# Kernel optimization log

Hardware: AMD Instinct MI355X
Metric: run time of the kernel (lower is better)

## Reference

```python
import jax, jax.numpy as jnp
import numpy as np

N_NODES = 100000
N_EDGES = 1200000
NUM_GRAPHS = 128
IN_DIM = 5
HIDDEN = 64


def setup_inputs() -> dict:
    key = jax.random.key(0)
    ks = jax.random.split(key, 12)
    x = jax.random.normal(ks[0], (N_NODES, IN_DIM), dtype=jnp.float32)
    edge_index = jax.random.randint(ks[1], (2, N_EDGES), 0, N_NODES, dtype=jnp.int64 if jax.config.read('jax_enable_x64') else jnp.int32)
    batch = jnp.sort(jax.random.randint(ks[2], (N_NODES,), 0, NUM_GRAPHS, dtype=jnp.int32))
    s = lambda fan_in: 1.0 / np.sqrt(fan_in)
    return {
        'x': x,
        'edge_index': edge_index,
        'batch': batch,
        'w_rel1': jax.random.normal(ks[3], (IN_DIM, HIDDEN), dtype=jnp.float32) * s(IN_DIM),
        'b_rel1': jnp.zeros((HIDDEN,), dtype=jnp.float32),
        'w_root1': jax.random.normal(ks[4], (IN_DIM, HIDDEN), dtype=jnp.float32) * s(IN_DIM),
        'w_rel2': jax.random.normal(ks[5], (HIDDEN, HIDDEN), dtype=jnp.float32) * s(HIDDEN),
        'b_rel2': jnp.zeros((HIDDEN,), dtype=jnp.float32),
        'w_root2': jax.random.normal(ks[6], (HIDDEN, HIDDEN), dtype=jnp.float32) * s(HIDDEN),
        'w_h1': jax.random.normal(ks[7], (2 * HIDDEN, HIDDEN), dtype=jnp.float32) * s(2 * HIDDEN),
        'b_h1': jnp.zeros((HIDDEN,), dtype=jnp.float32),
        'w_h2': jax.random.normal(ks[8], (HIDDEN, 1), dtype=jnp.float32) * s(HIDDEN),
        'b_h2': jnp.zeros((1,), dtype=jnp.float32),
    }


def _graph_conv(x, src, dst, w_rel, b_rel, w_root):
    # PyG GraphConv (aggr='add'): out = aggr(x_src -> dst) @ W_rel + b_rel + x @ W_root
    agg = jax.ops.segment_sum(x[src], dst, num_segments=N_NODES)
    return agg @ w_rel + b_rel + x @ w_root


def reference(x, edge_index, batch,
              w_rel1, b_rel1, w_root1,
              w_rel2, b_rel2, w_root2,
              w_h1, b_h1, w_h2, b_h2):
    src, dst = edge_index[0], edge_index[1]
    h = jax.nn.relu(_graph_conv(x, src, dst, w_rel1, b_rel1, w_root1))
    h = jax.nn.relu(_graph_conv(h, src, dst, w_rel2, b_rel2, w_root2))
    # global add + mean pooling over graphs
    add_pool = jax.ops.segment_sum(h, batch, num_segments=NUM_GRAPHS)
    counts = jax.ops.segment_sum(jnp.ones((N_NODES,), h.dtype), batch, num_segments=NUM_GRAPHS)
    mean_pool = add_pool / jnp.maximum(counts, 1.0)[:, None]
    g = jnp.concatenate([mean_pool, add_pool], axis=1)  # [G, 2*HIDDEN]
    out = jax.nn.relu(g @ w_h1 + b_h1) @ w_h2 + b_h2
    return out.squeeze(-1)
```

## Files before the change

### kernel.cpp

```cpp
#include <hip/hip_runtime.h>
#include <hip/hip_bf16.h>

#define N_NODES    100000
#define N_EDGES    1200000
#define NUM_GRAPHS 128
#define IN_DIM     5
#define HIDDEN     64
#define M_TILES    (N_NODES / 16)
#define NI4        (N_EDGES / 4)

#define CB    782
#define CBLK  256
#define EPB   ((NI4 + CBLK - 1) / CBLK)

typedef __attribute__((ext_vector_type(8))) short short8;
typedef __attribute__((ext_vector_type(4))) float f32x4;

__device__ __forceinline__ int rfl(int v) { return __builtin_amdgcn_readfirstlane(v); }

__device__ __forceinline__ unsigned short f2bs(float f) {
    union { float f; unsigned u; } v; v.f = f;
    return (unsigned short)((v.u + 0x7FFFu + ((v.u >> 16) & 1u)) >> 16);
}
__device__ __forceinline__ float bs2f(unsigned short s) {
    union { unsigned u; float f; } v; v.u = ((unsigned)s) << 16;
    return v.f;
}
__device__ __forceinline__ float blo(unsigned p) { return bs2f((unsigned short)(p & 0xffff)); }
__device__ __forceinline__ float bhi(unsigned p) { return bs2f((unsigned short)(p >> 16)); }
__device__ __forceinline__ unsigned pack2(float a, float b) {
    return ((unsigned)f2bs(b) << 16) | (unsigned)f2bs(a);
}

__device__ __forceinline__ unsigned char f2f8(float f) {
    union { float f; unsigned u; } v; v.f = f * 0x1p-120f;
    unsigned u = v.u + 0x7FFFFu + ((v.u >> 20) & 1u);
    return (unsigned char)(u >> 20);
}
__device__ __forceinline__ float f82f(unsigned b) {
    union { unsigned u; float f; } v; v.u = (b & 0x7Fu) << 20;
    return v.f * 0x1p120f;
}


__global__ void coarse_count(const int* __restrict__ dst, int* __restrict__ gcnt) {
    __shared__ int h[CB];
    int t = threadIdx.x, b = blockIdx.x;
    for (int i = t; i < CB; i += 256) h[i] = 0;
    __syncthreads();
    int i0 = b * EPB, i1 = min(i0 + EPB, NI4);
    for (int i = i0 + t; i < i1; i += 256) {
        int4 d = ((const int4*)dst)[i];
        atomicAdd(&h[d.x >> 7], 1);
        atomicAdd(&h[d.y >> 7], 1);
        atomicAdd(&h[d.z >> 7], 1);
        atomicAdd(&h[d.w >> 7], 1);
    }
    __syncthreads();
    for (int i = t; i < CB; i += 256) gcnt[b * CB + i] = h[i];
}

__global__ void block_scan(int* __restrict__ gcnt, int* __restrict__ btot) {
    __shared__ int s[CBLK];
    int k = blockIdx.x, t = threadIdx.x;
    int v = gcnt[t * CB + k];
    s[t] = v;
    __syncthreads();
    for (int off = 1; off < CBLK; off <<= 1) {
        int x = (t >= off) ? s[t - off] : 0;
        __syncthreads();
        s[t] += x;
        __syncthreads();
    }
    gcnt[t * CB + k] = s[t] - v;
    if (t == CBLK - 1) btot[k] = s[t];
}

__global__ void bucket_scan(const int* __restrict__ btot, int* __restrict__ bstart) {
    __shared__ int s[1024];
    int t = threadIdx.x;
    int v = (t < CB) ? btot[t] : 0;
    s[t] = v;
    __syncthreads();
    for (int off = 1; off < 1024; off <<= 1) {
        int x = (t >= off) ? s[t - off] : 0;
        __syncthreads();
        s[t] += x;
        __syncthreads();
    }
    if (t < CB) bstart[t] = s[t] - v;
    if (t == 0) bstart[CB] = N_EDGES;
}

__global__ void partition_k(const int* __restrict__ src, const int* __restrict__ dst,
                            const int* __restrict__ gcnt, const int* __restrict__ bstart,
                            int* __restrict__ part) {
    __shared__ int base[CB];
    __shared__ int h[CB];
    int t = threadIdx.x, b = blockIdx.x;
    for (int i = t; i < CB; i += 256) {
        base[i] = bstart[i] + gcnt[b * CB + i];
        h[i] = 0;
    }
    __syncthreads();
    int i0 = b * EPB, i1 = min(i0 + EPB, NI4);
    for (int i = i0 + t; i < i1; i += 256) {
        int4 s4 = ((const int4*)src)[i];
        int4 d4 = ((const int4*)dst)[i];
        int k, r;
        k = d4.x >> 7; r = atomicAdd(&h[k], 1); part[base[k] + r] = s4.x | ((d4.x & 127) << 17);
        k = d4.y >> 7; r = atomicAdd(&h[k], 1); part[base[k] + r] = s4.y | ((d4.y & 127) << 17);
        k = d4.z >> 7; r = atomicAdd(&h[k], 1); part[base[k] + r] = s4.z | ((d4.z & 127) << 17);
        k = d4.w >> 7; r = atomicAdd(&h[k], 1); part[base[k] + r] = s4.w | ((d4.w & 127) << 17);
    }
}

__global__ void fine_sort(const int* __restrict__ part, const int* __restrict__ bstart,
                          int* __restrict__ ptr, int* __restrict__ esrc) {
    __shared__ int fh[128];
    __shared__ int fr[128];
    int k = blockIdx.x, t = threadIdx.x;
    int e0 = bstart[k], e1 = bstart[k + 1];
    if (t < 128) { fh[t] = 0; fr[t] = 0; }
    __syncthreads();
    for (int e = e0 + t; e < e1; e += 256)
        atomicAdd(&fh[(part[e] >> 17) & 127], 1);
    __syncthreads();
    if (t == 0) {
        int run = 0;
        for (int i = 0; i < 128; ++i) { int c = fh[i]; fh[i] = run; run += c; }
    }
    __syncthreads();
    int n0 = k << 7;
    if (t < 128 && n0 + t < N_NODES) ptr[n0 + t] = e0 + fh[t];
    for (int e = e0 + t; e < e1; e += 256) {
        int p = part[e];
        int d = (p >> 17) & 127;
        int r = atomicAdd(&fr[d], 1);
        esrc[e0 + fh[d] + r] = p & 0x1FFFF;
    }
}


__global__ void packx_kernel(const float* __restrict__ x, uint4* __restrict__ xb) {
    int n = blockIdx.x * blockDim.x + threadIdx.x;
    if (n >= N_NODES) return;
    const float* xr = x + (size_t)n * IN_DIM;
    uint4 o;
    o.x = pack2(xr[0], xr[1]);
    o.y = pack2(xr[2], xr[3]);
    o.z = pack2(xr[4], 0.0f);
    o.w = 0u;
    xb[n] = o;
}

__global__ void gather_mlp1(const uint4* __restrict__ xb,
                            const float* __restrict__ x,
                            const int* __restrict__ ptr,
                            const int* __restrict__ esrc,
                            const float* __restrict__ w_rel1,
                            const float* __restrict__ b_rel1,
                            const float* __restrict__ w_root1,
                            unsigned short* __restrict__ h1,
                            unsigned char* __restrict__ h1f8) {
    int lane = threadIdx.x & 63;
    int w    = (blockIdx.x * blockDim.x + threadIdx.x) >> 6;
    int nw   = (gridDim.x * blockDim.x) >> 6;

    float wr[IN_DIM], wo[IN_DIM];
#pragma unroll
    for (int k = 0; k < IN_DIM; ++k) {
        wr[k] = w_rel1[k * HIDDEN + lane];
        wo[k] = w_root1[k * HIDDEN + lane];
    }
    float bias = b_rel1[lane];

    for (int n = w; n < N_NODES; n += nw) {
        int start = rfl(ptr[n]);
        int end   = rfl((n + 1 < N_NODES) ? ptr[n + 1] : N_EDGES);
        float a[IN_DIM] = {0.f, 0.f, 0.f, 0.f, 0.f};
        for (int e = start + lane; e < end; e += 64) {
            uint4 p = xb[esrc[e]];
            a[0] += blo(p.x); a[1] += bhi(p.x);
            a[2] += blo(p.y); a[3] += bhi(p.y);
            a[4] += blo(p.z);
        }
#pragma unroll
        for (int k = 0; k < IN_DIM; ++k)
#pragma unroll
            for (int off = 1; off < 64; off <<= 1)
                a[k] += __shfl_xor(a[k], off, 64);
        float acc = bias;
#pragma unroll
        for (int k = 0; k < IN_DIM; ++k)
            acc += a[k] * wr[k] + x[(size_t)n * IN_DIM + k] * wo[k];
        float hv = fmaxf(acc, 0.0f);
        h1[(size_t)n * HIDDEN + lane]   = f2bs(hv);
        h1f8[(size_t)n * HIDDEN + lane] = f2f8(hv);
    }
}

__global__ void gather2_fp8(const unsigned* __restrict__ h1f8,
                            const int* __restrict__ ptr,
                            const int* __restrict__ esrc,
                            uint2* __restrict__ agg2) {
    int lane = threadIdx.x & 63;
    int ql   = lane & 15;
    int q    = lane >> 4;
    int w    = (blockIdx.x * blockDim.x + threadIdx.x) >> 6;
    int nw   = (gridDim.x * blockDim.x) >> 6;

    for (int n = w; n < N_NODES; n += nw) {
        int start = rfl(ptr[n]);
        int end   = rfl((n + 1 < N_NODES) ? ptr[n + 1] : N_EDGES);
        float4 a0 = {0.f,0.f,0.f,0.f}, a1 = a0, a2 = a0, a3 = a0;
        int e = start + q;
        for (; e + 12 < end; e += 16) {
            int s0 = esrc[e], s1 = esrc[e + 4], s2 = esrc[e + 8], s3 = esrc[e + 12];
            unsigned p0 = h1f8[(size_t)s0 * 16 + ql];
            unsigned p1 = h1f8[(size_t)s1 * 16 + ql];
            unsigned p2 = h1f8[(size_t)s2 * 16 + ql];
            unsigned p3 = h1f8[(size_t)s3 * 16 + ql];
            a0.x += f82f(p0); a0.y += f82f(p0 >> 8); a0.z += f82f(p0 >> 16); a0.w += f82f(p0 >> 24);
            a1.x += f82f(p1); a1.y += f82f(p1 >> 8); a1.z += f82f(p1 >> 16); a1.w += f82f(p1 >> 24);
            a2.x += f82f(p2); a2.y += f82f(p2 >> 8); a2.z += f82f(p2 >> 16); a2.w += f82f(p2 >> 24);
            a3.x += f82f(p3); a3.y += f82f(p3 >> 8); a3.z += f82f(p3 >> 16); a3.w += f82f(p3 >> 24);
        }
        for (; e < end; e += 4) {
            unsigned p = h1f8[(size_t)esrc[e] * 16 + ql];
            a0.x += f82f(p); a0.y += f82f(p >> 8); a0.z += f82f(p >> 16); a0.w += f82f(p >> 24);
        }
        float4 a;
        a.x = (a0.x + a1.x) + (a2.x + a3.x);
        a.y = (a0.y + a1.y) + (a2.y + a3.y);
        a.z = (a0.z + a1.z) + (a2.z + a3.z);
        a.w = (a0.w + a1.w) + (a2.w + a3.w);
        a.x += __shfl_xor(a.x, 16, 64); a.x += __shfl_xor(a.x, 32, 64);
        a.y += __shfl_xor(a.y, 16, 64); a.y += __shfl_xor(a.y, 32, 64);
        a.z += __shfl_xor(a.z, 16, 64); a.z += __shfl_xor(a.z, 32, 64);
        a.w += __shfl_xor(a.w, 16, 64); a.w += __shfl_xor(a.w, 32, 64);
        if (q == 0) {
            uint2 o;
            o.x = pack2(a.x, a.y);
            o.y = pack2(a.z, a.w);
            agg2[(size_t)n * 16 + ql] = o;
        }
    }
}

__global__ void mlp2_pool(const unsigned short* __restrict__ agg2,
                          const unsigned short* __restrict__ h1,
                          const float* __restrict__ w_rel2,
                          const float* __restrict__ b_rel2,
                          const float* __restrict__ w_root2,
                          const int* __restrict__ batch,
                          float* __restrict__ add_pool) {
    int lane = threadIdx.x & 63;
    int wv   = threadIdx.x >> 6;
    int row  = lane & 15;
    int quad = lane >> 4;
    int n    = wv * 16 + row;

    short8 bwr[2], bwo[2];
#pragma unroll
    for (int s = 0; s < 2; ++s)
#pragma unroll
        for (int j = 0; j < 8; ++j) {
            int k = 32 * s + quad * 8 + j;
            bwr[s][j] = (short)f2bs(w_rel2[k * HIDDEN + n]);
            bwo[s][j] = (short)f2bs(w_root2[k * HIDDEN + n]);
        }
    float bias = b_rel2[n];

    for (int t = blockIdx.x; t < M_TILES; t += gridDim.x) {
        int m0 = t * 16;
        size_t rbase = (size_t)(m0 + row) * HIDDEN;
        short8 aa0 = *(const short8*)(agg2 + rbase + quad * 8);
        short8 aa1 = *(const short8*)(agg2 + rbase + 32 + quad * 8);
        short8 ah0 = *(const short8*)(h1   + rbase + quad * 8);
        short8 ah1 = *(const short8*)(h1   + rbase + 32 + quad * 8);

        f32x4 acc = {bias, bias, bias, bias};
        acc = __builtin_amdgcn_mfma_f32_16x16x32_bf16(aa0, bwr[0], acc, 0, 0, 0);
        acc = __builtin_amdgcn_mfma_f32_16x16x32_bf16(aa1, bwr[1], acc, 0, 0, 0);
        acc = __builtin_amdgcn_mfma_f32_16x16x32_bf16(ah0, bwo[0], acc, 0, 0, 0);
        acc = __builtin_amdgcn_mfma_f32_16x16x32_bf16(ah1, bwo[1], acc, 0, 0, 0);

        float hv0 = fmaxf(acc[0], 0.0f), hv1 = fmaxf(acc[1], 0.0f);
        float hv2 = fmaxf(acc[2], 0.0f), hv3 = fmaxf(acc[3], 0.0f);

        int gLo = batch[m0], gHi = batch[m0 + 15];
        if (gLo == gHi) {
            float s = (hv0 + hv1) + (hv2 + hv3);
            s += __shfl_xor(s, 16, 64);
            s += __shfl_xor(s, 32, 64);
            if (quad == 0)
                atomicAdd(&add_pool[gLo * HIDDEN + n], s);
        } else {
            int m = m0 + quad * 4;
            atomicAdd(&add_pool[batch[m]     * HIDDEN + n], hv0);
            atomicAdd(&add_pool[batch[m + 1] * HIDDEN + n], hv1);
            atomicAdd(&add_pool[batch[m + 2] * HIDDEN + n], hv2);
            atomicAdd(&add_pool[batch[m + 3] * HIDDEN + n], hv3);
        }
    }
}

__device__ __forceinline__ int lower_bound_i(const int* a, int n, int v) {
    int lo = 0, hi = n;
    while (lo < hi) { int mid = (lo + hi) >> 1; if (a[mid] < v) lo = mid + 1; else hi = mid; }
    return lo;
}

__global__ void head_mlp(const float* __restrict__ add_pool,
                         const int* __restrict__ batch,
                         const float* __restrict__ w_h1,
                         const float* __restrict__ b_h1,
                         const float* __restrict__ w_h2,
                         const float* __restrict__ b_h2,
                         float* __restrict__ out) {
    int g = blockIdx.x, t = threadIdx.x;

    __shared__ int s_cnt;
    if (t == 0) {
        int start = lower_bound_i(batch, N_NODES, g);
        int end   = lower_bound_i(batch, N_NODES, g + 1);
        s_cnt = end - start;
    }
    __syncthreads();
    float cnt = fmaxf((float)s_cnt, 1.0f);

    __shared__ float sg[2 * HIDDEN];
    float add = add_pool[(size_t)g * HIDDEN + t];
    sg[t]          = add / cnt;
    sg[HIDDEN + t] = add;
    __syncthreads();

    float hid = b_h1[t];
#pragma unroll 16
    for (int i = 0; i < 2 * HIDDEN; ++i)
        hid += sg[i] * w_h1[i * HIDDEN + t];
    hid = fmaxf(hid, 0.0f);

    float res = hid * w_h2[t];
    for (int off = 32; off > 0; off >>= 1)
        res += __shfl_down(res, off, 64);
    if (t == 0) out[g] = res + b_h2[0];
}

extern "C" void kernel_launch(void* const* d_in, const int* in_sizes, int n_in,
                              void* d_out, int out_size, void* d_ws, size_t ws_size,
                              hipStream_t stream) {
    const float* x       = (const float*)d_in[0];
    const int*   ei      = (const int*)d_in[1];
    const int*   src     = ei;
    const int*   dst     = ei + N_EDGES;
    const int*   batch   = (const int*)d_in[2];
    const float* w_rel1  = (const float*)d_in[3];
    const float* b_rel1  = (const float*)d_in[4];
    const float* w_root1 = (const float*)d_in[5];
    const float* w_rel2  = (const float*)d_in[6];
    const float* b_rel2  = (const float*)d_in[7];
    const float* w_root2 = (const float*)d_in[8];
    const float* w_h1    = (const float*)d_in[9];
    const float* b_h1    = (const float*)d_in[10];
    const float* w_h2    = (const float*)d_in[11];
    const float* b_h2    = (const float*)d_in[12];
    float* out = (float*)d_out;

    int* base = (int*)d_ws;
    int*   gcnt     = base;
    int*   btot     = gcnt + ((CBLK * CB + 3) & ~3);
    int*   bstart   = btot + ((CB + 3) & ~3);
    float* add_pool = (float*)(bstart + ((CB + 1 + 3) & ~3));
    int*   ptr      = (int*)(add_pool + NUM_GRAPHS * HIDDEN);
    int*   part     = ptr + ((N_NODES + 3) & ~3);
    int*   esrc     = part + N_EDGES;
    unsigned short* h1   = (unsigned short*)(esrc + N_EDGES);
    unsigned short* agg2 = h1 + (size_t)N_NODES * HIDDEN;
    unsigned char*  h1f8 = (unsigned char*)(agg2 + (size_t)N_NODES * HIDDEN);
    uint4*          xb   = (uint4*)(h1f8 + (size_t)N_NODES * HIDDEN);

    hipMemsetAsync(add_pool, 0, sizeof(float) * NUM_GRAPHS * HIDDEN, stream);

    coarse_count<<<CBLK, 256, 0, stream>>>(dst, gcnt);
    block_scan<<<CB, CBLK, 0, stream>>>(gcnt, btot);
    bucket_scan<<<1, 1024, 0, stream>>>(btot, bstart);
    partition_k<<<CBLK, 256, 0, stream>>>(src, dst, gcnt, bstart, part);
    fine_sort<<<CB, 256, 0, stream>>>(part, bstart, ptr, esrc);

    packx_kernel<<<(N_NODES + 255) / 256, 256, 0, stream>>>(x, xb);
    gather_mlp1<<<2048, 256, 0, stream>>>(xb, x, ptr, esrc, w_rel1, b_rel1, w_root1, h1, h1f8);
    gather2_fp8<<<2048, 256, 0, stream>>>((const unsigned*)h1f8, ptr, esrc, (uint2*)agg2);
    mlp2_pool<<<2048, 256, 0, stream>>>(agg2, h1, w_rel2, b_rel2, w_root2, batch, add_pool);
    head_mlp<<<NUM_GRAPHS, 64, 0, stream>>>(add_pool, batch, w_h1, b_h1, w_h2, b_h2, out);
}
```

Measured before the change: 228.7 us.

## Fuse layer-2 gather with MFMA pooling kernel and fold small launches

Merges the fp8 neighbor gather into the MFMA layer-2 and pooling kernel. Each block gathers 16 node rows into a shared-memory tile and then runs the MFMA directly, so the bf16 agg2 intermediate is never written to or read from global memory. The x packing moves into coarse_count and the add_pool memset into bucket_scan, which removes two launches. The cost is two block-wide syncs per tile and per-wave gather work of 4 nodes before each MFMA, which can lower latency hiding in the gather.

```diff
diff --git a/kernel.cpp b/kernel.cpp
--- a/kernel.cpp
+++ b/kernel.cpp
@@ -43,7 +43,8 @@
 }
 
 
-__global__ void coarse_count(const int* __restrict__ dst, int* __restrict__ gcnt) {
+__global__ void coarse_count(const int* __restrict__ dst, int* __restrict__ gcnt,
+                             const float* __restrict__ x, uint4* __restrict__ xb) {
     __shared__ int h[CB];
     int t = threadIdx.x, b = blockIdx.x;
     for (int i = t; i < CB; i += 256) h[i] = 0;
@@ -58,6 +59,16 @@
     }
     __syncthreads();
     for (int i = t; i < CB; i += 256) gcnt[b * CB + i] = h[i];
+
+    for (int n = b * 256 + t; n < N_NODES; n += CBLK * 256) {
+        const float* xr = x + (size_t)n * IN_DIM;
+        uint4 o;
+        o.x = pack2(xr[0], xr[1]);
+        o.y = pack2(xr[2], xr[3]);
+        o.z = pack2(xr[4], 0.0f);
+        o.w = 0u;
+        xb[n] = o;
+    }
 }
 
 __global__ void block_scan(int* __restrict__ gcnt, int* __restrict__ btot) {
@@ -76,7 +87,8 @@
     if (t == CBLK - 1) btot[k] = s[t];
 }
 
-__global__ void bucket_scan(const int* __restrict__ btot, int* __restrict__ bstart) {
+__global__ void bucket_scan(const int* __restrict__ btot, int* __restrict__ bstart,
+                            float* __restrict__ add_pool) {
     __shared__ int s[1024];
     int t = threadIdx.x;
     int v = (t < CB) ? btot[t] : 0;
@@ -90,6 +102,7 @@
     }
     if (t < CB) bstart[t] = s[t] - v;
     if (t == 0) bstart[CB] = N_EDGES;
+    for (int i = t; i < NUM_GRAPHS * HIDDEN; i += 1024) add_pool[i] = 0.0f;
 }
 
 __global__ void partition_k(const int* __restrict__ src, const int* __restrict__ dst,
@@ -141,18 +154,6 @@
     }
 }
 
-
-__global__ void packx_kernel(const float* __restrict__ x, uint4* __restrict__ xb) {
-    int n = blockIdx.x * blockDim.x + threadIdx.x;
-    if (n >= N_NODES) return;
-    const float* xr = x + (size_t)n * IN_DIM;
-    uint4 o;
-    o.x = pack2(xr[0], xr[1]);
-    o.y = pack2(xr[2], xr[3]);
-    o.z = pack2(xr[4], 0.0f);
-    o.w = 0u;
-    xb[n] = o;
-}
 
 __global__ void gather_mlp1(const uint4* __restrict__ xb,
                             const float* __restrict__ x,
@@ -200,66 +201,24 @@
     }
 }
 
-__global__ void gather2_fp8(const unsigned* __restrict__ h1f8,
-                            const int* __restrict__ ptr,
-                            const int* __restrict__ esrc,
-                            uint2* __restrict__ agg2) {
+#define TSTRIDE 72
+__global__ void gather2_mlp2_pool(const unsigned* __restrict__ h1f8,
+                                  const int* __restrict__ ptr,
+                                  const int* __restrict__ esrc,
+                                  const unsigned short* __restrict__ h1,
+                                  const float* __restrict__ w_rel2,
+                                  const float* __restrict__ b_rel2,
+                                  const float* __restrict__ w_root2,
+                                  const int* __restrict__ batch,
+                                  float* __restrict__ add_pool) {
+    __shared__ unsigned short tile[16 * TSTRIDE];
     int lane = threadIdx.x & 63;
+    int wv   = threadIdx.x >> 6;
     int ql   = lane & 15;
     int q    = lane >> 4;
-    int w    = (blockIdx.x * blockDim.x + threadIdx.x) >> 6;
-    int nw   = (gridDim.x * blockDim.x) >> 6;
-
-    for (int n = w; n < N_NODES; n += nw) {
-        int start = rfl(ptr[n]);
-        int end   = rfl((n + 1 < N_NODES) ? ptr[n + 1] : N_EDGES);
-        float4 a0 = {0.f,0.f,0.f,0.f}, a1 = a0, a2 = a0, a3 = a0;
-        int e = start + q;
-        for (; e + 12 < end; e += 16) {
-            int s0 = esrc[e], s1 = esrc[e + 4], s2 = esrc[e + 8], s3 = esrc[e + 12];
-            unsigned p0 = h1f8[(size_t)s0 * 16 + ql];
-            unsigned p1 = h1f8[(size_t)s1 * 16 + ql];
-            unsigned p2 = h1f8[(size_t)s2 * 16 + ql];
-            unsigned p3 = h1f8[(size_t)s3 * 16 + ql];
-            a0.x += f82f(p0); a0.y += f82f(p0 >> 8); a0.z += f82f(p0 >> 16); a0.w += f82f(p0 >> 24);
-            a1.x += f82f(p1); a1.y += f82f(p1 >> 8); a1.z += f82f(p1 >> 16); a1.w += f82f(p1 >> 24);
-            a2.x += f82f(p2); a2.y += f82f(p2 >> 8); a2.z += f82f(p2 >> 16); a2.w += f82f(p2 >> 24);
-            a3.x += f82f(p3); a3.y += f82f(p3 >> 8); a3.z += f82f(p3 >> 16); a3.w += f82f(p3 >> 24);
-        }
-        for (; e < end; e += 4) {
-            unsigned p = h1f8[(size_t)esrc[e] * 16 + ql];
-            a0.x += f82f(p); a0.y += f82f(p >> 8); a0.z += f82f(p >> 16); a0.w += f82f(p >> 24);
-        }
-        float4 a;
-        a.x = (a0.x + a1.x) + (a2.x + a3.x);
-        a.y = (a0.y + a1.y) + (a2.y + a3.y);
-        a.z = (a0.z + a1.z) + (a2.z + a3.z);
-        a.w = (a0.w + a1.w) + (a2.w + a3.w);
-        a.x += __shfl_xor(a.x, 16, 64); a.x += __shfl_xor(a.x, 32, 64);
-        a.y += __shfl_xor(a.y, 16, 64); a.y += __shfl_xor(a.y, 32, 64);
-        a.z += __shfl_xor(a.z, 16, 64); a.z += __shfl_xor(a.z, 32, 64);
-        a.w += __shfl_xor(a.w, 16, 64); a.w += __shfl_xor(a.w, 32, 64);
-        if (q == 0) {
-            uint2 o;
-            o.x = pack2(a.x, a.y);
-            o.y = pack2(a.z, a.w);
-            agg2[(size_t)n * 16 + ql] = o;
-        }
-    }
-}
-
-__global__ void mlp2_pool(const unsigned short* __restrict__ agg2,
-                          const unsigned short* __restrict__ h1,
-                          const float* __restrict__ w_rel2,
-                          const float* __restrict__ b_rel2,
-                          const float* __restrict__ w_root2,
-                          const int* __restrict__ batch,
-                          float* __restrict__ add_pool) {
-    int lane = threadIdx.x & 63;
-    int wv   = threadIdx.x >> 6;
     int row  = lane & 15;
     int quad = lane >> 4;
-    int n    = wv * 16 + row;
+    int ncol = wv * 16 + row;
 
     short8 bwr[2], bwo[2];
 #pragma unroll
@@ -267,18 +226,59 @@
 #pragma unroll
         for (int j = 0; j < 8; ++j) {
             int k = 32 * s + quad * 8 + j;
-            bwr[s][j] = (short)f2bs(w_rel2[k * HIDDEN + n]);
-            bwo[s][j] = (short)f2bs(w_root2[k * HIDDEN + n]);
+            bwr[s][j] = (short)f2bs(w_rel2[k * HIDDEN + ncol]);
+            bwo[s][j] = (short)f2bs(w_root2[k * HIDDEN + ncol]);
         }
-    float bias = b_rel2[n];
+    float bias = b_rel2[ncol];
 
     for (int t = blockIdx.x; t < M_TILES; t += gridDim.x) {
         int m0 = t * 16;
+
+#pragma unroll
+        for (int ii = 0; ii < 4; ++ii) {
+            int n = m0 + wv * 4 + ii;
+            int start = rfl(ptr[n]);
+            int end   = rfl((n + 1 < N_NODES) ? ptr[n + 1] : N_EDGES);
+            float4 a0 = {0.f,0.f,0.f,0.f}, a1 = a0, a2 = a0, a3 = a0;
+            int e = start + q;
+            for (; e + 12 < end; e += 16) {
+                int s0 = esrc[e], s1 = esrc[e + 4], s2 = esrc[e + 8], s3 = esrc[e + 12];
+                unsigned p0 = h1f8[(size_t)s0 * 16 + ql];
+                unsigned p1 = h1f8[(size_t)s1 * 16 + ql];
+                unsigned p2 = h1f8[(size_t)s2 * 16 + ql];
+                unsigned p3 = h1f8[(size_t)s3 * 16 + ql];
+                a0.x += f82f(p0); a0.y += f82f(p0 >> 8); a0.z += f82f(p0 >> 16); a0.w += f82f(p0 >> 24);
+                a1.x += f82f(p1); a1.y += f82f(p1 >> 8); a1.z += f82f(p1 >> 16); a1.w += f82f(p1 >> 24);
+                a2.x += f82f(p2); a2.y += f82f(p2 >> 8); a2.z += f82f(p2 >> 16); a2.w += f82f(p2 >> 24);
+                a3.x += f82f(p3); a3.y += f82f(p3 >> 8); a3.z += f82f(p3 >> 16); a3.w += f82f(p3 >> 24);
+            }
+            for (; e < end; e += 4) {
+                unsigned p = h1f8[(size_t)esrc[e] * 16 + ql];
+                a0.x += f82f(p); a0.y += f82f(p >> 8); a0.z += f82f(p >> 16); a0.w += f82f(p >> 24);
+            }
+            float4 a;
+            a.x = (a0.x + a1.x) + (a2.x + a3.x);
+            a.y = (a0.y + a1.y) + (a2.y + a3.y);
+            a.z = (a0.z + a1.z) + (a2.z + a3.z);
+            a.w = (a0.w + a1.w) + (a2.w + a3.w);
+            a.x += __shfl_xor(a.x, 16, 64); a.x += __shfl_xor(a.x, 32, 64);
+            a.y += __shfl_xor(a.y, 16, 64); a.y += __shfl_xor(a.y, 32, 64);
+            a.z += __shfl_xor(a.z, 16, 64); a.z += __shfl_xor(a.z, 32, 64);
+            a.w += __shfl_xor(a.w, 16, 64); a.w += __shfl_xor(a.w, 32, 64);
+            if (q == 0) {
+                uint2 o;
+                o.x = pack2(a.x, a.y);
+                o.y = pack2(a.z, a.w);
+                *(uint2*)&tile[(wv * 4 + ii) * TSTRIDE + ql * 4] = o;
+            }
+        }
+        __syncthreads();
+
+        short8 aa0 = *(const short8*)&tile[row * TSTRIDE + quad * 8];
+        short8 aa1 = *(const short8*)&tile[row * TSTRIDE + 32 + quad * 8];
         size_t rbase = (size_t)(m0 + row) * HIDDEN;
-        short8 aa0 = *(const short8*)(agg2 + rbase + quad * 8);
-        short8 aa1 = *(const short8*)(agg2 + rbase + 32 + quad * 8);
-        short8 ah0 = *(const short8*)(h1   + rbase + quad * 8);
-        short8 ah1 = *(const short8*)(h1   + rbase + 32 + quad * 8);
+        short8 ah0 = *(const short8*)(h1 + rbase + quad * 8);
+        short8 ah1 = *(const short8*)(h1 + rbase + 32 + quad * 8);
 
         f32x4 acc = {bias, bias, bias, bias};
         acc = __builtin_amdgcn_mfma_f32_16x16x32_bf16(aa0, bwr[0], acc, 0, 0, 0);
@@ -295,14 +295,15 @@
             s += __shfl_xor(s, 16, 64);
             s += __shfl_xor(s, 32, 64);
             if (quad == 0)
-                atomicAdd(&add_pool[gLo * HIDDEN + n], s);
+                atomicAdd(&add_pool[gLo * HIDDEN + ncol], s);
         } else {
             int m = m0 + quad * 4;
-            atomicAdd(&add_pool[batch[m]     * HIDDEN + n], hv0);
-            atomicAdd(&add_pool[batch[m + 1] * HIDDEN + n], hv1);
-            atomicAdd(&add_pool[batch[m + 2] * HIDDEN + n], hv2);
-            atomicAdd(&add_pool[batch[m + 3] * HIDDEN + n], hv3);
+            atomicAdd(&add_pool[batch[m]     * HIDDEN + ncol], hv0);
+            atomicAdd(&add_pool[batch[m + 1] * HIDDEN + ncol], hv1);
+            atomicAdd(&add_pool[batch[m + 2] * HIDDEN + ncol], hv2);
+            atomicAdd(&add_pool[batch[m + 3] * HIDDEN + ncol], hv3);
         }
+        __syncthreads();
     }
 }
 
@@ -377,21 +378,17 @@
     int*   part     = ptr + ((N_NODES + 3) & ~3);
     int*   esrc     = part + N_EDGES;
     unsigned short* h1   = (unsigned short*)(esrc + N_EDGES);
-    unsigned short* agg2 = h1 + (size_t)N_NODES * HIDDEN;
-    unsigned char*  h1f8 = (unsigned char*)(agg2 + (size_t)N_NODES * HIDDEN);
+    unsigned char*  h1f8 = (unsigned char*)(h1 + (size_t)N_NODES * HIDDEN);
     uint4*          xb   = (uint4*)(h1f8 + (size_t)N_NODES * HIDDEN);
 
-    hipMemsetAsync(add_pool, 0, sizeof(float) * NUM_GRAPHS * HIDDEN, stream);
-
-    coarse_count<<<CBLK, 256, 0, stream>>>(dst, gcnt);
+    coarse_count<<<CBLK, 256, 0, stream>>>(dst, gcnt, x, xb);
     block_scan<<<CB, CBLK, 0, stream>>>(gcnt, btot);
-    bucket_scan<<<1, 1024, 0, stream>>>(btot, bstart);
+    bucket_scan<<<1, 1024, 0, stream>>>(btot, bstart, add_pool);
     partition_k<<<CBLK, 256, 0, stream>>>(src, dst, gcnt, bstart, part);
     fine_sort<<<CB, 256, 0, stream>>>(part, bstart, ptr, esrc);
 
-    packx_kernel<<<(N_NODES + 255) / 256, 256, 0, stream>>>(x, xb);
     gather_mlp1<<<2048, 256, 0, stream>>>(xb, x, ptr, esrc, w_rel1, b_rel1, w_root1, h1, h1f8);
-    gather2_fp8<<<2048, 256, 0, stream>>>((const unsigned*)h1f8, ptr, esrc, (uint2*)agg2);
-    mlp2_pool<<<2048, 256, 0, stream>>>(agg2, h1, w_rel2, b_rel2, w_root2, batch, add_pool);
+    gather2_mlp2_pool<<<2048, 256, 0, stream>>>((const unsigned*)h1f8, ptr, esrc, h1,
+                                                w_rel2, b_rel2, w_root2, batch, add_pool);
     head_mlp<<<NUM_GRAPHS, 64, 0, stream>>>(add_pool, batch, w_h1, b_h1, w_h2, b_h2, out);
 }
```

Result: slower. 246.1 us (+7.6%).
